# Kernel optimization log

Hardware: AMD Instinct MI355X
Metric: run time of the kernel (lower is better)

Reference implementation:

```python
import jax, jax.numpy as jnp
import numpy as np

EMB = 512
NUM_HEAD = 8
HEAD_DIM = EMB // NUM_HEAD  # 64
B, S = 16, 2048


def setup_inputs() -> dict:
    key = jax.random.key(0)
    k1, k2, k3, k4 = jax.random.split(key, 4)
    x1 = jax.random.normal(k1, (B, S, EMB), dtype=jnp.float32)
    # causal mask: 1 where attention allowed, 0 elsewhere (masked_fill where mask==0)
    mask = jnp.tril(jnp.ones((S, S), dtype=jnp.int32))
    scale = 1.0 / np.sqrt(EMB)
    Wq = jax.random.normal(k2, (EMB, HEAD_DIM), dtype=jnp.float32) * scale
    Wk = jax.random.normal(k3, (EMB, HEAD_DIM), dtype=jnp.float32) * scale
    Wv = jax.random.normal(k4, (EMB, HEAD_DIM), dtype=jnp.float32) * scale
    return {"x1": x1, "mask": mask, "Wq": Wq, "Wk": Wk, "Wv": Wv}


def reference(x1, mask, Wq, Wk, Wv):
    # q,k,v: [B,S,H]
    q = jnp.einsum('bse,eh->bsh', x1, Wq)
    k = jnp.einsum('bse,eh->bsh', x1, Wk)
    v = jnp.einsum('bse,eh->bsh', x1, Wv)
    # scores: [B,S,S]
    scaled_qk = jnp.einsum('bqh,bkh->bqk', q, k) / jnp.sqrt(jnp.float32(HEAD_DIM))
    scaled_qk = jnp.where(mask == 0, -jnp.inf, scaled_qk)
    attn = jax.nn.softmax(scaled_qk, axis=-1)
    return jnp.einsum('bqk,bkh->bqh', attn, v)
```

## Files before the change

kernel.cpp:

```cpp
#include <hip/hip_runtime.h>
#include <hip/hip_bf16.h>

typedef __attribute__((ext_vector_type(8))) short bf16x8;
typedef __attribute__((ext_vector_type(4))) float f32x4;
typedef __attribute__((ext_vector_type(4))) unsigned short u16x4;

#define MFMA16(a, b, c) __builtin_amdgcn_mfma_f32_16x16x32_bf16(a, b, c, 0, 0, 0)

#define QSCALE 0.18033688011112042f

#define GLDS16(gp, lp)                                                         \
    __builtin_amdgcn_global_load_lds(                                          \
        (const __attribute__((address_space(1))) void*)(gp),                   \
        (__attribute__((address_space(3))) void*)(lp), 16, 0, 0)

__device__ __forceinline__ short nbf(float f) {
    __hip_bfloat16 h = __float2bfloat16(f);
    return *(short*)&h;
}
__device__ __forceinline__ unsigned short nbfu(float f) {
    __hip_bfloat16 h = __float2bfloat16(f);
    return *(unsigned short*)&h;
}

__global__ void wt_kernel(const float* __restrict__ Wq, const float* __restrict__ Wk,
                          const float* __restrict__ Wv, unsigned short* __restrict__ Wt) {
    const int h = blockIdx.x;
    const int mat = blockIdx.y;
    const int e = threadIdx.x;
    const float* W = (mat == 0) ? Wq : ((mat == 1) ? Wk : Wv);
    Wt[(mat * 64 + h) * 512 + e] = nbfu(W[e * 64 + h]);
}

__global__ __launch_bounds__(512, 1) void qkv_proj(
    const float* __restrict__ x1, const unsigned short* __restrict__ Wt,
    unsigned short* __restrict__ Q, unsigned short* __restrict__ K,
    unsigned short* __restrict__ Vt)
{
    __shared__ char alds[2][16384];
    __shared__ char blds[2][12288];

    const int tid = threadIdx.x;
    const int W = tid >> 6, lane = tid & 63;
    const int c = lane & 15, g = lane >> 4;
    const int tokB = blockIdx.x * 128;

    const char* x1b = (const char*)x1;
    const char* Wtb = (const char*)Wt;

    const int tA0 = tid >> 3,           qA0 = (tid & 7) ^ (tA0 & 7);
    const int tA1 = (tid + 512) >> 3,   qA1 = (tid & 7) ^ (tA1 & 7);
    const size_t aoff0 = (size_t)(tokB + tA0) * 2048 + qA0 * 16;
    const size_t aoff1 = (size_t)(tokB + tA1) * 2048 + qA1 * 16;

    auto bsrc = [&](int j) -> size_t {
        const int n = j >> 6, c2 = (j >> 2) & 15, g2 = j & 3;
        return (size_t)((n >> 2) * 64 + (n & 3) * 16 + c2) * 1024 + g2 * 16;
    };
    const size_t boff0 = bsrc(tid), boff1 = bsrc(tid + 512);

    f32x4 acc[12];
#pragma unroll
    for (int n = 0; n < 12; ++n) acc[n] = (f32x4)0.f;

    GLDS16(x1b + aoff0, &alds[0][tid * 16]);
    GLDS16(x1b + aoff1, &alds[0][8192 + tid * 16]);
    GLDS16(Wtb + boff0, &blds[0][tid * 16]);
    if (tid < 256) GLDS16(Wtb + boff1, &blds[0][8192 + tid * 16]);

    const int arow = (W * 16 + c) * 128;
    const int aq0 = (((2 * g) ^ (c & 7)) * 16);
    const int aq1 = (((2 * g + 1) ^ (c & 7)) * 16);
    const int brd = (c * 4 + g) * 16;

    int buf = 0;
    for (int ks = 0; ks < 16; ++ks) {
        asm volatile("s_waitcnt vmcnt(0)\n\ts_barrier" ::: "memory");

        if (ks < 15) {
            const size_t ka = (size_t)(ks + 1) * 128;
            const size_t kb = (size_t)(ks + 1) * 64;
            char* ab = &alds[buf ^ 1][0];
            char* bb = &blds[buf ^ 1][0];
            GLDS16(x1b + aoff0 + ka, ab + tid * 16);
            GLDS16(x1b + aoff1 + ka, ab + 8192 + tid * 16);
            GLDS16(Wtb + boff0 + kb, bb + tid * 16);
            if (tid < 256) GLDS16(Wtb + boff1 + kb, bb + 8192 + tid * 16);
        }

        const char* ab = &alds[buf][0];
        const char* bb = &blds[buf][0];
        f32x4 a0 = *(const f32x4*)(ab + arow + aq0);
        f32x4 a1 = *(const f32x4*)(ab + arow + aq1);
        bf16x8 af;
        af[0] = nbf(a0[0]); af[1] = nbf(a0[1]); af[2] = nbf(a0[2]); af[3] = nbf(a0[3]);
        af[4] = nbf(a1[0]); af[5] = nbf(a1[1]); af[6] = nbf(a1[2]); af[7] = nbf(a1[3]);
#pragma unroll
        for (int n = 0; n < 12; ++n) {
            bf16x8 bf = *(const bf16x8*)(bb + n * 1024 + brd);
            acc[n] = MFMA16(af, bf, acc[n]);
        }
        buf ^= 1;
    }

    const int tok0 = tokB + W * 16;
#pragma unroll
    for (int n = 0; n < 4; ++n)
#pragma unroll
        for (int r = 0; r < 4; ++r)
            Q[(size_t)(tok0 + g * 4 + r) * 64 + n * 16 + c] = nbfu(acc[n][r] * QSCALE);
#pragma unroll
    for (int n = 0; n < 4; ++n)
#pragma unroll
        for (int r = 0; r < 4; ++r)
            K[(size_t)(tok0 + g * 4 + r) * 64 + n * 16 + c] = nbfu(acc[4 + n][r]);

    const int b = tok0 >> 11;
    const int sl = (tok0 & 2047) + g * 4;
#pragma unroll
    for (int n = 0; n < 4; ++n) {
        const int d = n * 16 + c;
        u16x4 pv;
#pragma unroll
        for (int r = 0; r < 4; ++r) pv[r] = nbfu(acc[8 + n][r]);
        *(u16x4*)(Vt + ((size_t)(b * 64 + d) << 11) + sl) = pv;
    }
}

__global__ __launch_bounds__(512, 2) void flash_attn(
    const unsigned short* __restrict__ Q, const unsigned short* __restrict__ K,
    const unsigned short* __restrict__ Vt, float* __restrict__ out)
{
    __shared__ char kv[2][65536];
    __shared__ char p_lds[32768];

    const int tid = threadIdx.x;
    const int W = tid >> 6;
    const int st = W >> 2;
    const int w = W & 3;
    const int lane = tid & 63;
    const int c = lane & 15, g = lane >> 4;

    const int id = blockIdx.x;
    const int b = 2 * (id & 7) + ((id >> 3) & 1);
    const int qt = 31 - (id >> 4);
    const int n2 = (qt >> 1) + 1;
    const int J = (n2 + 1) >> 1;
    const int qr0c = qt * 64 + w * 16 + c;
    const size_t qrow_g = ((size_t)b << 11) + qt * 64 + w * 16;

    bf16x8 qf0 = *(const bf16x8*)(Q + (qrow_g + c) * 64 + g * 8);
    bf16x8 qf1 = *(const bf16x8*)(Q + (qrow_g + c) * 64 + 32 + g * 8);

    const char* Kb = (const char*)(K + (((size_t)b << 11) * 64));
    const char* Vb = (const char*)(Vt + (((size_t)b << 11) * 64));

    const int c2 = tid & 15, g2 = (tid >> 4) & 3, nn = (tid >> 6) & 3, s4 = (tid >> 8) & 1;
    const int koff = (nn * 16 + c2) * 128 + g2 * 16 + s4 * 64;
    const int voff = (nn * 16 + c2) * 4096 + g2 * 16 + s4 * 64;

    float m = -1e30f, l = 0.f;
    f32x4 acc[4];
#pragma unroll
    for (int n = 0; n < 4; ++n) acc[n] = (f32x4)0.f;

    {
        char* d = &kv[0][0];
        GLDS16(Kb + koff,                 d + tid * 16);
        GLDS16(Kb + koff + 8192,          d + 8192 + tid * 16);
        GLDS16(Vb + voff,                 d + 16384 + tid * 16);
        GLDS16(Vb + voff + 128,           d + 16384 + 8192 + tid * 16);
        GLDS16(Kb + 16384 + koff,         d + 32768 + tid * 16);
        GLDS16(Kb + 16384 + koff + 8192,  d + 32768 + 8192 + tid * 16);
        GLDS16(Vb + 256 + voff,           d + 49152 + tid * 16);
        GLDS16(Vb + 256 + voff + 128,     d + 49152 + 8192 + tid * 16);
    }

    for (int j = 0; j < J; ++j) {
        asm volatile("s_waitcnt vmcnt(0)\n\ts_barrier" ::: "memory");

        if (j + 1 < J) {
            const size_t kA = (size_t)(2 * j + 2) * 16384;
            const size_t vA = (size_t)(2 * j + 2) * 256;
            char* d = &kv[(j & 1) ^ 1][0];
            GLDS16(Kb + kA + koff,                 d + tid * 16);
            GLDS16(Kb + kA + koff + 8192,          d + 8192 + tid * 16);
            GLDS16(Vb + vA + voff,                 d + 16384 + tid * 16);
            GLDS16(Vb + vA + voff + 128,           d + 16384 + 8192 + tid * 16);
            GLDS16(Kb + kA + 16384 + koff,         d + 32768 + tid * 16);
            GLDS16(Kb + kA + 16384 + koff + 8192,  d + 32768 + 8192 + tid * 16);
            GLDS16(Vb + vA + 256 + voff,           d + 49152 + tid * 16);
            GLDS16(Vb + vA + 256 + voff + 128,     d + 49152 + 8192 + tid * 16);
        }

        const int t = 2 * j + st;
        if (t < n2) {
            const char* kb = &kv[j & 1][st * 32768];
            const char* vb = kb + 16384;

            bf16x8 kfA[8], kfB[8];
#pragma unroll
            for (int h = 0; h < 2; ++h)
#pragma unroll
                for (int n = 0; n < 4; ++n) {
                    kfA[h * 4 + n] = *(const bf16x8*)(kb + h * 8192 + n * 1024 + lane * 16);
                    kfB[h * 4 + n] = *(const bf16x8*)(kb + h * 8192 + 4096 + n * 1024 + lane * 16);
                }
            bf16x8 vf[16];
#pragma unroll
            for (int ps = 0; ps < 4; ++ps)
#pragma unroll
                for (int n = 0; n < 4; ++n)
                    vf[ps * 4 + n] = *(const bf16x8*)(vb + (ps >> 1) * 8192 + (ps & 1) * 4096 + n * 1024 + lane * 16);

            f32x4 s[8];
#pragma unroll
            for (int i = 0; i < 8; ++i) s[i] = (f32x4)0.f;
            __builtin_amdgcn_s_setprio(1);
#pragma unroll
            for (int i = 0; i < 8; ++i) {
                s[i] = MFMA16(kfA[i], qf0, s[i]);
                s[i] = MFMA16(kfB[i], qf1, s[i]);
            }
            __builtin_amdgcn_s_setprio(0);

            if (t == n2 - 1) {
#pragma unroll
                for (int h = 0; h < 2; ++h)
#pragma unroll
                    for (int n = 0; n < 4; ++n) {
                        const int key0 = t * 128 + h * 64 + n * 16 + g * 4;
#pragma unroll
                        for (int r = 0; r < 4; ++r)
                            if (key0 + r > qr0c) s[h * 4 + n][r] = -1e30f;
                    }
            }

            float tm = -1e30f;
#pragma unroll
            for (int i = 0; i < 8; ++i)
                tm = fmaxf(tm, fmaxf(fmaxf(s[i][0], s[i][1]), fmaxf(s[i][2], s[i][3])));

            if (__any(tm > m + 8.f)) {
                float gm = tm;
                gm = fmaxf(gm, __shfl_xor(gm, 16, 64));
                gm = fmaxf(gm, __shfl_xor(gm, 32, 64));
                const float mn = fmaxf(m, gm);
                const float alpha = exp2f(m - mn);
                m = mn;
                l *= alpha;
                float al[4];
#pragma unroll
                for (int r = 0; r < 4; ++r) al[r] = __shfl(alpha, g * 4 + r, 16);
#pragma unroll
                for (int n = 0; n < 4; ++n)
#pragma unroll
                    for (int r = 0; r < 4; ++r) acc[n][r] *= al[r];
            }

            char* pw = &p_lds[W * 4096 + ((g >> 1) * 16 + c) * 16 + (g & 1) * 8];
#pragma unroll
            for (int h = 0; h < 2; ++h)
#pragma unroll
                for (int n = 0; n < 4; ++n) {
                    const int i = h * 4 + n;
                    float p0 = exp2f(s[i][0] - m);
                    float p1 = exp2f(s[i][1] - m);
                    float p2 = exp2f(s[i][2] - m);
                    float p3 = exp2f(s[i][3] - m);
                    l += (p0 + p1) + (p2 + p3);
                    u16x4 pk;
                    pk[0] = nbfu(p0); pk[1] = nbfu(p1); pk[2] = nbfu(p2); pk[3] = nbfu(p3);
                    *(u16x4*)(pw + (h * 2 + (n >> 1)) * 1024 + (n & 1) * 512) = pk;
                }

            const char* pr = &p_lds[W * 4096 + lane * 16];
            bf16x8 pf[4];
#pragma unroll
            for (int ps = 0; ps < 4; ++ps) pf[ps] = *(const bf16x8*)(pr + ps * 1024);

            __builtin_amdgcn_s_setprio(1);
#pragma unroll
            for (int n = 0; n < 4; ++n)
#pragma unroll
                for (int ps = 0; ps < 4; ++ps)
                    acc[n] = MFMA16(pf[ps], vf[ps * 4 + n], acc[n]);
            __builtin_amdgcn_s_setprio(0);
        }
    }

    __syncthreads();
    float* accb = (float*)&kv[0][0];
    float* mb = (float*)&kv[0][16384];
    float* lb = (float*)&kv[0][16384 + 256];

    if (st == 1) {
        l += __shfl_xor(l, 16, 64);
        l += __shfl_xor(l, 32, 64);
        if (g == 0) { mb[w * 16 + c] = m; lb[w * 16 + c] = l; }
#pragma unroll
        for (int n = 0; n < 4; ++n)
#pragma unroll
            for (int r = 0; r < 4; ++r)
                accb[w * 1024 + (g * 4 + r) * 64 + n * 16 + c] = acc[n][r];
    }
    __syncthreads();

    if (st == 0) {
        l += __shfl_xor(l, 16, 64);
        l += __shfl_xor(l, 32, 64);
        const float m1c = mb[w * 16 + c];
        const float l1c = lb[w * 16 + c];
        const float mF = fmaxf(m, m1c);
        const float a0 = exp2f(m - mF);
        const float a1 = (m1c > -1e29f) ? exp2f(m1c - mF) : 0.f;
        const float inv = 1.f / (l * a0 + l1c * a1);
        const float s0 = a0 * inv, s1 = a1 * inv;
        float s0r[4], s1r[4];
#pragma unroll
        for (int r = 0; r < 4; ++r) {
            s0r[r] = __shfl(s0, g * 4 + r, 16);
            s1r[r] = __shfl(s1, g * 4 + r, 16);
        }
#pragma unroll
        for (int n = 0; n < 4; ++n)
#pragma unroll
            for (int r = 0; r < 4; ++r) {
                const float a1v = accb[w * 1024 + (g * 4 + r) * 64 + n * 16 + c];
                out[(qrow_g + g * 4 + r) * 64 + n * 16 + c] = acc[n][r] * s0r[r] + a1v * s1r[r];
            }
    }
}

extern "C" void kernel_launch(void* const* d_in, const int* in_sizes, int n_in,
                              void* d_out, int out_size, void* d_ws, size_t ws_size,
                              hipStream_t stream) {
    const float* x1 = (const float*)d_in[0];
    const float* Wq = (const float*)d_in[2];
    const float* Wk = (const float*)d_in[3];
    const float* Wv = (const float*)d_in[4];
    float* out = (float*)d_out;

    unsigned short* Wt  = (unsigned short*)d_ws;
    unsigned short* Qw  = (unsigned short*)((char*)d_ws + 196608);
    unsigned short* Kw  = (unsigned short*)((char*)d_ws + 196608 + 4194304);
    unsigned short* Vtw = (unsigned short*)((char*)d_ws + 196608 + 2 * 4194304);

    wt_kernel<<<dim3(64, 3), 512, 0, stream>>>(Wq, Wk, Wv, Wt);
    qkv_proj<<<256, 512, 0, stream>>>(x1, Wt, Qw, Kw, Vtw);
    flash_attn<<<512, 512, 0, stream>>>(Qw, Kw, Vtw, out);
}
```

Before: 65.82 us.

## Defer PV MFMA for second key-tile stream into next iteration with register-held V

```diff
diff --git a/kernel.cpp b/kernel.cpp
--- a/kernel.cpp
+++ b/kernel.cpp
@@ -163,6 +163,8 @@
     f32x4 acc[4];
 #pragma unroll
     for (int n = 0; n < 4; ++n) acc[n] = (f32x4)0.f;
+
+    bf16x8 vfd[16];
 
     {
         char* d = &kv[0][0];
@@ -177,7 +179,7 @@
     }
 
     for (int j = 0; j < J; ++j) {
-        asm volatile("s_waitcnt vmcnt(0)\n\ts_barrier" ::: "memory");
+        asm volatile("s_waitcnt vmcnt(0) lgkmcnt(0)\n\ts_barrier" ::: "memory");
 
         if (j + 1 < J) {
             const size_t kA = (size_t)(2 * j + 2) * 16384;
@@ -193,6 +195,20 @@
             GLDS16(Vb + vA + 256 + voff + 128,     d + 49152 + 8192 + tid * 16);
         }
 
+        if (st == 1 && j >= 1) {
+            const char* pr = &p_lds[W * 4096 + lane * 16];
+            bf16x8 pf[4];
+#pragma unroll
+            for (int ps = 0; ps < 4; ++ps) pf[ps] = *(const bf16x8*)(pr + ps * 1024);
+            __builtin_amdgcn_s_setprio(1);
+#pragma unroll
+            for (int n = 0; n < 4; ++n)
+#pragma unroll
+                for (int ps = 0; ps < 4; ++ps)
+                    acc[n] = MFMA16(pf[ps], vfd[ps * 4 + n], acc[n]);
+            __builtin_amdgcn_s_setprio(0);
+        }
+
         const int t = 2 * j + st;
         if (t < n2) {
             const char* kb = &kv[j & 1][st * 32768];
@@ -206,13 +222,6 @@
                     kfA[h * 4 + n] = *(const bf16x8*)(kb + h * 8192 + n * 1024 + lane * 16);
                     kfB[h * 4 + n] = *(const bf16x8*)(kb + h * 8192 + 4096 + n * 1024 + lane * 16);
                 }
-            bf16x8 vf[16];
-#pragma unroll
-            for (int ps = 0; ps < 4; ++ps)
-#pragma unroll
-                for (int n = 0; n < 4; ++n)
-                    vf[ps * 4 + n] = *(const bf16x8*)(vb + (ps >> 1) * 8192 + (ps & 1) * 4096 + n * 1024 + lane * 16);
-
             f32x4 s[8];
 #pragma unroll
             for (int i = 0; i < 8; ++i) s[i] = (f32x4)0.f;
@@ -274,19 +283,40 @@
                     *(u16x4*)(pw + (h * 2 + (n >> 1)) * 1024 + (n & 1) * 512) = pk;
                 }
 
-            const char* pr = &p_lds[W * 4096 + lane * 16];
-            bf16x8 pf[4];
-#pragma unroll
-            for (int ps = 0; ps < 4; ++ps) pf[ps] = *(const bf16x8*)(pr + ps * 1024);
-
-            __builtin_amdgcn_s_setprio(1);
-#pragma unroll
-            for (int n = 0; n < 4; ++n)
+            if (st == 0) {
+                const char* pr = &p_lds[W * 4096 + lane * 16];
+                bf16x8 pf[4];
+#pragma unroll
+                for (int ps = 0; ps < 4; ++ps) pf[ps] = *(const bf16x8*)(pr + ps * 1024);
+                __builtin_amdgcn_s_setprio(1);
+#pragma unroll
+                for (int n = 0; n < 4; ++n)
+#pragma unroll
+                    for (int ps = 0; ps < 4; ++ps) {
+                        bf16x8 vf = *(const bf16x8*)(vb + (ps >> 1) * 8192 + (ps & 1) * 4096 + n * 1024 + lane * 16);
+                        acc[n] = MFMA16(pf[ps], vf, acc[n]);
+                    }
+                __builtin_amdgcn_s_setprio(0);
+            } else {
 #pragma unroll
                 for (int ps = 0; ps < 4; ++ps)
-                    acc[n] = MFMA16(pf[ps], vf[ps * 4 + n], acc[n]);
-            __builtin_amdgcn_s_setprio(0);
-        }
+#pragma unroll
+                    for (int n = 0; n < 4; ++n)
+                        vfd[ps * 4 + n] = *(const bf16x8*)(vb + (ps >> 1) * 8192 + (ps & 1) * 4096 + n * 1024 + lane * 16);
+            }
+        }
+    }
+
+    if (st == 1 && (2 * J - 1) < n2) {
+        const char* pr = &p_lds[W * 4096 + lane * 16];
+        bf16x8 pf[4];
+#pragma unroll
+        for (int ps = 0; ps < 4; ++ps) pf[ps] = *(const bf16x8*)(pr + ps * 1024);
+#pragma unroll
+        for (int n = 0; n < 4; ++n)
+#pragma unroll
+            for (int ps = 0; ps < 4; ++ps)
+                acc[n] = MFMA16(pf[ps], vfd[ps * 4 + n], acc[n]);
     }
 
     __syncthreads();
```

Measured after the change: 66.03 us. No clear change (+0.3%).
